# Performance work log

Measured on AMD Instinct MI355X. Metric: run time of the kernel, lower is better.

## Reference

```python
import jax, jax.numpy as jnp
import numpy as np

DECAY = 0.99
EPSILON = 1e-05
BETA = 0.25  # vq_commitment_beta


def setup_inputs() -> dict:
    key = jax.random.key(0)
    k1, k2, k3, k4 = jax.random.split(key, 4)
    N, dim, K = 32768, 512, 8192
    init_range = 1.0 / np.sqrt(dim)
    emb_w = jax.random.uniform(k3, (K, 2 * dim), dtype=jnp.float32,
                               minval=-init_range, maxval=init_range)
    return {
        "z_real": jax.random.normal(k1, (N, dim), dtype=jnp.float32),
        "z_imag": jax.random.normal(k2, (N, dim), dtype=jnp.float32),
        "emb_w": emb_w,
        "ema_cluster_size": jnp.zeros((K,), dtype=jnp.float32),
        "ema_w": emb_w.copy(),
    }


def reference(z_real, z_imag, emb_w, ema_cluster_size, ema_w):
    N, dim = z_real.shape
    K = emb_w.shape[0]
    z_flat = jnp.concatenate([z_real, z_imag], axis=-1)  # [N, 2*dim]

    # squared euclidean distances [N, K]
    x_sq = jnp.sum(z_flat * z_flat, axis=1, keepdims=True)
    y_sq = jnp.sum(emb_w * emb_w, axis=1)
    d = jnp.maximum(x_sq + y_sq - 2.0 * (z_flat @ emb_w.T), 0.0)
    indices = jnp.argmin(d, axis=-1)  # [N]
    z_q = emb_w[indices]              # [N, 2*dim]

    # EMA codebook update (training-mode buffer math, no grads)
    n_total = jnp.zeros((K,), z_flat.dtype).at[indices].add(1.0)
    new_cluster_size = ema_cluster_size * DECAY + (1.0 - DECAY) * n_total
    cs = new_cluster_size + EPSILON
    cs = cs + (cs < 1.0).astype(cs.dtype)
    dw = jnp.zeros((K, 2 * dim), z_flat.dtype).at[indices].add(z_flat)  # encodings.T @ z_flat
    new_ema_w = ema_w * DECAY + (1.0 - DECAY) * dw
    new_w = jnp.clip(new_ema_w / cs[:, None], -5.0, 5.0)

    loss_sample = BETA * jnp.mean((z_q - z_flat) ** 2, axis=-1)  # [N]

    # straight-through (forward value == z_q)
    z_q_st = z_flat + jax.lax.stop_gradient(z_q - z_flat)

    probs = n_total / N
    norm_entropy = -jnp.sum(probs * jnp.log(probs + 1e-10)) / np.log(float(K))

    z_q_r = z_q_st[..., :dim]
    z_q_i = z_q_st[..., dim:]
    return (z_q_r, z_q_i, loss_sample, indices, norm_entropy,
            new_w, new_cluster_size, new_ema_w)
```

## Files before the change

### kernel.cpp

```cpp
#include <hip/hip_runtime.h>
#include <hip/hip_bf16.h>

#define NROWS 32768
#define DIM   512
#define D2    1024
#define KCODE 8192
#define DECAYF 0.99f
#define OMD    0.01f
#define CANDCAP 16
#define ZMAX 6.0f
#define IRANGE 0.04419417382415922f
#define MARGIN_P (9200 << 7)

typedef __attribute__((ext_vector_type(4))) int   v4i;
typedef __attribute__((ext_vector_type(16))) int  i32x16;

#define WS_EMB8T   0u
#define WS_YSQ     8388608u
#define WS_NINT    8421376u
#define WS_ENT     8454144u
#define WS_FIDX    10682384u
#define WS_OFF     10813456u
#define WS_CUR     10846224u
#define WS_ROWLIST 10878992u

#define OUT_ZQR  0
#define OUT_ZQI  16777216
#define OUT_LOSS 33554432
#define OUT_IDX  33587200
#define OUT_ENT  33619968
#define OUT_NEWW 33619969
#define OUT_NCS  42008577
#define OUT_NEMA 42016769
#define PAIRS_OFF (OUT_NEWW + 1)

__device__ __forceinline__ float wredf(float v) {
    #pragma unroll
    for (int o = 32; o > 0; o >>= 1) v += __shfl_down(v, o, 64);
    return v;
}

__device__ __forceinline__ double wredd(double v) {
    #pragma unroll
    for (int o = 32; o > 0; o >>= 1) v += __shfl_down(v, o, 64);
    return __shfl(v, 0, 64);
}

__device__ __forceinline__ double ulp32_of(double v) {
    return scalbn(1.0, ilogb(v) - 23);
}

__device__ __forceinline__ void gload_lds16(const void* g, void* l) {
    __builtin_amdgcn_global_load_lds(
        (const __attribute__((address_space(1))) unsigned int*)(g),
        (__attribute__((address_space(3))) unsigned int*)(l), 16, 0, 0);
}

__device__ __forceinline__ int q4(float4 v, float s) {
    int a = (int)rintf(fminf(fmaxf(v.x * s, -127.f), 127.f));
    int b = (int)rintf(fminf(fmaxf(v.y * s, -127.f), 127.f));
    int c = (int)rintf(fminf(fmaxf(v.z * s, -127.f), 127.f));
    int d = (int)rintf(fminf(fmaxf(v.w * s, -127.f), 127.f));
    return (a & 255) | ((b & 255) << 8) | ((c & 255) << 16) | ((d & 255) << 24);
}

__global__ __launch_bounds__(256) void prep_emb(const float* __restrict__ emb,
                                                char* __restrict__ emb8t,
                                                int* __restrict__ ysq) {
    int wave = threadIdx.x >> 6, lane = threadIdx.x & 63;
    int k = blockIdx.x * 4 + wave;
    const float4* src = (const float4*)(emb + (size_t)k * D2);
    const float es = 127.0f / IRANGE;
    const float sfac_inv = 1.0f / (2.0f * (ZMAX / 127.0f) * (IRANGE / 127.0f));
    float s = 0.f;
    float4 v0 = src[lane * 4 + 0];
    float4 v1 = src[lane * 4 + 1];
    float4 v2 = src[lane * 4 + 2];
    float4 v3 = src[lane * 4 + 3];
    s += v0.x*v0.x + v0.y*v0.y + v0.z*v0.z + v0.w*v0.w;
    s += v1.x*v1.x + v1.y*v1.y + v1.z*v1.z + v1.w*v1.w;
    s += v2.x*v2.x + v2.y*v2.y + v2.z*v2.z + v2.w*v2.w;
    s += v3.x*v3.x + v3.y*v3.y + v3.z*v3.z + v3.w*v3.w;
    v4i pk; pk[0] = q4(v0, es); pk[1] = q4(v1, es); pk[2] = q4(v2, es); pk[3] = q4(v3, es);
    v4i* dst = (v4i*)(emb8t + (size_t)(k >> 5) * 32768 + (size_t)lane * 512 + (k & 31) * 16);
    *dst = pk;
    s = wredf(s);
    if (lane == 0) ysq[k] = (int)rintf(s * sfac_inv);
}

__global__ __launch_bounds__(256, 2) void argmin_gemm(
    const float* __restrict__ zr, const float* __restrict__ zi,
    const char* __restrict__ emb8t, const int* __restrict__ ysq,
    long long* __restrict__ pairs)
{
    __shared__ char bufs[2][32768];
    const int tid  = threadIdx.x;
    const int wave = tid >> 6, lane = tid & 63;
    const int colc = lane & 31;
    const int hh   = lane >> 5;
    const int rowblk = blockIdx.x >> 1;
    const int slice  = blockIdx.x & 1;

    const int arow = rowblk * 128 + wave * 32 + colc;
    const float zs = 127.0f / ZMAX;
    const float* zrp = zr + (size_t)arow * 512 + hh * 16;
    const float* zip = zi + (size_t)arow * 512 + hh * 16;
    v4i afrag[32];
    #pragma unroll
    for (int ft = 0; ft < 16; ++ft) {
        const float4* p = (const float4*)(zrp + ft * 32);
        v4i a; a[0] = q4(p[0], zs); a[1] = q4(p[1], zs); a[2] = q4(p[2], zs); a[3] = q4(p[3], zs);
        afrag[ft] = a;
    }
    #pragma unroll
    for (int ft = 0; ft < 16; ++ft) {
        const float4* p = (const float4*)(zip + ft * 32);
        v4i a; a[0] = q4(p[0], zs); a[1] = q4(p[1], zs); a[2] = q4(p[2], zs); a[3] = q4(p[3], zs);
        afrag[16 + ft] = a;
    }

    int tv0[16], tv1[16];
    #pragma unroll
    for (int g = 0; g < 16; ++g) { tv0[g] = 0x7FFFFFFF; tv1[g] = 0x7FFFFFFF; }

    const char* gslice = emb8t + (size_t)slice * 128 * 32768;
    const int* yslice = ysq + slice * 4096;

#define STAGE(dstbuf, t_) do {                                                   \
        const char* gb = gslice + (size_t)(t_) * 32768 + wave * 8192             \
                       + (size_t)lane * 16;                                      \
        char* lb = (dstbuf) + wave * 8192;                                       \
        _Pragma("unroll")                                                        \
        for (int q = 0; q < 8; ++q)                                              \
            gload_lds16(gb + q * 1024, lb + q * 1024);                           \
    } while (0)

    const int boff = colc * 16 + hh * 512;

    STAGE(bufs[0], 0);
    __syncthreads();

    for (int c = 0; c < 128; ++c) {
        const int cur = c & 1;
        if (c + 1 < 128) STAGE(bufs[cur ^ 1], c + 1);
        int ysv = yslice[c * 32 + colc];

        const char* bb = &bufs[cur][0] + boff;
        i32x16 accP, accQ;
        #pragma unroll
        for (int g = 0; g < 16; ++g) { accP[g] = 0; accQ[g] = 0; }
        __builtin_amdgcn_s_setprio(1);
        #pragma unroll
        for (int m = 0; m < 16; ++m) {
            v4i bP = *(const v4i*)(bb + (2 * m) * 1024);
            v4i bQ = *(const v4i*)(bb + (2 * m + 1) * 1024);
            accP = __builtin_amdgcn_mfma_i32_32x32x32_i8(afrag[2 * m],     bP, accP, 0, 0, 0);
            accQ = __builtin_amdgcn_mfma_i32_32x32x32_i8(afrag[2 * m + 1], bQ, accQ, 0, 0, 0);
        }
        __builtin_amdgcn_s_setprio(0);

        #pragma unroll
        for (int g = 0; g < 16; ++g) {
            int pk = ((ysv - accP[g] - accQ[g]) << 7) | c;
            tv1[g] = min(tv1[g], max(pk, tv0[g]));
            tv0[g] = min(tv0[g], pk);
        }
        __syncthreads();
    }
#undef STAGE

    #pragma unroll
    for (int g = 0; g < 16; ++g) {
        int rloc = (g & 3) + 8 * (g >> 2) + 4 * hh;
        int rowg = rowblk * 128 + wave * 32 + rloc;
        size_t base = (size_t)rowg * 128 + slice * 64 + colc * 2;
        int t0 = tv0[g], t1 = tv1[g];
        int code0 = slice * 4096 + (t0 & 127) * 32 + colc;
        int code1 = slice * 4096 + (t1 & 127) * 32 + colc;
        pairs[base + 0] = ((long long)(unsigned)code0 << 32) | (unsigned)t0;
        pairs[base + 1] = ((long long)(unsigned)code1 << 32) | (unsigned)t1;
    }
}

__global__ __launch_bounds__(256) void cleanup(
    const float* __restrict__ zr, const float* __restrict__ zi,
    const float* __restrict__ emb, const long long* __restrict__ pairs,
    int* __restrict__ fidx, int* __restrict__ nint, float* __restrict__ out)
{
    __shared__ int candlds[4][CANDCAP];
    int wave = threadIdx.x >> 6, lane = threadIdx.x & 63;
    int r = blockIdx.x * 4 + wave;

    const long long* pr = pairs + (size_t)r * 128;
    long long p0 = pr[lane];
    long long p1 = pr[64 + lane];
    int v0v = (int)(unsigned)p0;
    int i0  = (int)(p0 >> 32);
    int v1v = (int)(unsigned)p1;
    int i1  = (int)(p1 >> 32);
    int m = min(v0v, v1v);
    #pragma unroll
    for (int o = 32; o > 0; o >>= 1) m = min(m, __shfl_xor(m, o, 64));
    int lim = m + MARGIN_P;
    unsigned long long m0 = __ballot(v0v < lim);
    unsigned long long m1 = __ballot(v1v < lim);
    int t0 = __popcll(m0);
    int cnt = t0 + __popcll(m1);
    if (cnt > CANDCAP) cnt = CANDCAP;
    unsigned long long below = (lane == 63) ? 0xFFFFFFFFFFFFFFFFull >> 1
                                            : ((1ull << lane) - 1);
    if (v0v < lim) {
        int pos = __popcll(m0 & below);
        if (pos < CANDCAP) candlds[wave][pos] = i0;
    }
    if (v1v < lim) {
        int pos = t0 + __popcll(m1 & below);
        if (pos < CANDCAP) candlds[wave][pos] = i1;
    }
    int best = candlds[wave][0];

    float zreg[16];
    #pragma unroll
    for (int p = 0; p < 4; ++p) {
        int d4 = p * 64 + lane;
        const float4* zp = (d4 < 128) ? (const float4*)(zr + (size_t)r * 512)
                                      : ((const float4*)(zi + (size_t)r * 512) - 128);
        float4 zv = zp[d4];
        zreg[p * 4 + 0] = zv.x; zreg[p * 4 + 1] = zv.y;
        zreg[p * 4 + 2] = zv.z; zreg[p * 4 + 3] = zv.w;
    }

    if (cnt > 1) {
        double xs = 0.0;
        #pragma unroll
        for (int j = 0; j < 16; ++j) xs += (double)zreg[j] * (double)zreg[j];
        xs = wredd(xs);
        double uS = ulp32_of(xs);

        double bD = 1e300; int bi = 1 << 30;
        for (int i = 0; i < cnt; ++i) {
            int cdx = candlds[wave][i];
            const float4* ep = (const float4*)(emb + (size_t)cdx * 1024);
            double ys = 0.0, tt = 0.0;
            #pragma unroll
            for (int p = 0; p < 4; ++p) {
                float4 ev = ep[p * 64 + lane];
                float q0 = ev.x * ev.x, q1 = ev.y * ev.y, q2 = ev.z * ev.z, q3 = ev.w * ev.w;
                ys += (double)q0 + (double)q1 + (double)q2 + (double)q3;
                tt += (double)zreg[p * 4 + 0] * (double)ev.x
                    + (double)zreg[p * 4 + 1] * (double)ev.y
                    + (double)zreg[p * 4 + 2] * (double)ev.z
                    + (double)zreg[p * 4 + 3] * (double)ev.w;
            }
            ys = wredd(ys);
            tt = wredd(tt);
            float y32 = (float)ys;
            float t32 = (float)tt;
            double dex = xs + ys - 2.0 * tt;
            double ud = ulp32_of(dex);
            double D = rint((double)y32 / uS) * uS - rint(2.0 * (double)t32 / ud) * ud;
            if (D < bD || (D == bD && cdx < bi)) { bD = D; bi = cdx; }
        }
        best = bi;
    }

    const float4* ep = (const float4*)(emb + (size_t)best * 1024);
    float acc = 0.f;
    #pragma unroll
    for (int p = 0; p < 4; ++p) {
        int d4 = p * 64 + lane;
        float4 ev = ep[d4];
        float dx = ev.x - zreg[p * 4 + 0]; acc += dx * dx;
        float dy = ev.y - zreg[p * 4 + 1]; acc += dy * dy;
        float dz = ev.z - zreg[p * 4 + 2]; acc += dz * dz;
        float dw = ev.w - zreg[p * 4 + 3]; acc += dw * dw;
        float4* op = (d4 < 128) ? (float4*)(out + OUT_ZQR + (size_t)r * 512)
                                : ((float4*)(out + OUT_ZQI + (size_t)r * 512) - 128);
        op[d4] = ev;
    }
    acc = wredf(acc);
    if (lane == 0) {
        fidx[r] = best;
        out[OUT_IDX + r] = (float)best;
        out[OUT_LOSS + r] = 0.25f * acc * (1.f / 1024.f);
        atomicAdd(nint + best, 1);
    }
}

__global__ __launch_bounds__(256) void scan_codes(const int* __restrict__ nint,
                                                  int* __restrict__ off,
                                                  int* __restrict__ cur) {
    __shared__ int part[256];
    int tid = threadIdx.x;
    int base = tid * 32;
    int loc[32];
    int s = 0;
    #pragma unroll
    for (int j = 0; j < 32; ++j) { loc[j] = s; s += nint[base + j]; }
    part[tid] = s;
    __syncthreads();
    for (int o = 1; o < 256; o <<= 1) {
        int t = (tid >= o) ? part[tid - o] : 0;
        __syncthreads();
        part[tid] += t;
        __syncthreads();
    }
    int excl = part[tid] - s;
    #pragma unroll
    for (int j = 0; j < 32; ++j) {
        off[base + j] = excl + loc[j];
        cur[base + j] = 0;
    }
}

__global__ __launch_bounds__(256) void fill_rows(const int* __restrict__ fidx,
                                                 const int* __restrict__ off,
                                                 int* __restrict__ cur,
                                                 int* __restrict__ rowlist) {
    int r = blockIdx.x * 256 + threadIdx.x;
    int idx = fidx[r];
    int pos = atomicAdd(cur + idx, 1);
    rowlist[off[idx] + pos] = r;
}

__global__ __launch_bounds__(256) void ema_update(
    const float* __restrict__ zr, const float* __restrict__ zi,
    const float* __restrict__ emaw, const float* __restrict__ emacs,
    const int* __restrict__ nint, const int* __restrict__ off,
    const int* __restrict__ rowlist, float* __restrict__ out,
    float* __restrict__ entacc)
{
    int k = blockIdx.x;
    int tid = threadIdx.x;
    int cnt = nint[k];
    int o0 = off[k];
    float ax = 0.f, ay = 0.f, az = 0.f, aw = 0.f;
    for (int i = 0; i < cnt; ++i) {
        int r = rowlist[o0 + i];
        float4 zv = (tid < 128) ? ((const float4*)(zr + (size_t)r * 512))[tid]
                                : ((const float4*)(zi + (size_t)r * 512))[tid - 128];
        ax += zv.x; ay += zv.y; az += zv.z; aw += zv.w;
    }
    float4 ew = ((const float4*)(emaw + (size_t)k * 1024))[tid];
    float4 nem;
    nem.x = DECAYF * ew.x + OMD * ax;
    nem.y = DECAYF * ew.y + OMD * ay;
    nem.z = DECAYF * ew.z + OMD * az;
    nem.w = DECAYF * ew.w + OMD * aw;
    ((float4*)(out + OUT_NEMA + (size_t)k * 1024))[tid] = nem;
    float ncs = DECAYF * emacs[k] + OMD * (float)cnt;
    float cs = ncs + 1e-5f;
    if (cs < 1.f) cs += 1.f;
    float inv = 1.f / cs;
    float4 w;
    w.x = fminf(fmaxf(nem.x * inv, -5.f), 5.f);
    w.y = fminf(fmaxf(nem.y * inv, -5.f), 5.f);
    w.z = fminf(fmaxf(nem.z * inv, -5.f), 5.f);
    w.w = fminf(fmaxf(nem.w * inv, -5.f), 5.f);
    ((float4*)(out + OUT_NEWW + (size_t)k * 1024))[tid] = w;
    if (tid == 0) {
        out[OUT_NCS + k] = ncs;
        float p = (float)cnt / 32768.f;
        atomicAdd(entacc, -p * logf(p + 1e-10f));
    }
}

__global__ void ent_fin(const float* __restrict__ entacc, float* __restrict__ out) {
    if (threadIdx.x == 0) out[OUT_ENT] = entacc[0] / logf(8192.f);
}

extern "C" void kernel_launch(void* const* d_in, const int* in_sizes, int n_in,
                              void* d_out, int out_size, void* d_ws, size_t ws_size,
                              hipStream_t stream)
{
    const float* zr    = (const float*)d_in[0];
    const float* zi    = (const float*)d_in[1];
    const float* emb   = (const float*)d_in[2];
    const float* emacs = (const float*)d_in[3];
    const float* emaw  = (const float*)d_in[4];
    float* out = (float*)d_out;
    char* ws = (char*)d_ws;

    char*  emb8t   = (char*)(ws + WS_EMB8T);
    int*   ysq     = (int*)(ws + WS_YSQ);
    int*   nint    = (int*)(ws + WS_NINT);
    float* entacc  = (float*)(ws + WS_ENT);
    int*   fidx    = (int*)(ws + WS_FIDX);
    int*   off     = (int*)(ws + WS_OFF);
    int*   cur     = (int*)(ws + WS_CUR);
    int*   rowlist = (int*)(ws + WS_ROWLIST);
    long long* pairs = (long long*)(out + PAIRS_OFF);

    hipMemsetAsync(ws + WS_NINT, 0, 32768 + 16, stream);

    prep_emb   <<<2048, 256, 0, stream>>>(emb, emb8t, ysq);
    argmin_gemm<<<512,  256, 0, stream>>>(zr, zi, emb8t, ysq, pairs);
    cleanup    <<<8192, 256, 0, stream>>>(zr, zi, emb, pairs, fidx, nint, out);
    scan_codes <<<1,    256, 0, stream>>>(nint, off, cur);
    fill_rows  <<<128,  256, 0, stream>>>(fidx, off, cur, rowlist);
    ema_update <<<8192, 256, 0, stream>>>(zr, zi, emaw, emacs, nint, off, rowlist, out, entacc);
    ent_fin    <<<1,    64,  0, stream>>>(entacc, out);
}
```

Before: 545.5 us.

## Double rows per wave in int8 argmin GEMM and fold memset into prep

Each wave now handles 64 query rows (two 32-row A fragments) against every staged codebook tile, so each LDS B read feeds twice as many MFMAs. The grid halves to 256 blocks and launch bounds drop to one block per CU to make room for the doubled A fragments, accumulators and top-2 trackers. The separate memset of the count and entropy buffers is folded into prep_emb, removing one launch. The cost is heavy register pressure and only 256 blocks, which may leave CUs underused or cause spills.

```diff
diff --git a/kernel.cpp b/kernel.cpp
--- a/kernel.cpp
+++ b/kernel.cpp
@@ -66,7 +66,12 @@
 
 __global__ __launch_bounds__(256) void prep_emb(const float* __restrict__ emb,
                                                 char* __restrict__ emb8t,
-                                                int* __restrict__ ysq) {
+                                                int* __restrict__ ysq,
+                                                int* __restrict__ nint,
+                                                float* __restrict__ entacc) {
+    if (blockIdx.x < 32) nint[blockIdx.x * 256 + threadIdx.x] = 0;
+    else if (blockIdx.x == 32 && threadIdx.x == 0) entacc[0] = 0.f;
+
     int wave = threadIdx.x >> 6, lane = threadIdx.x & 63;
     int k = blockIdx.x * 4 + wave;
     const float4* src = (const float4*)(emb + (size_t)k * D2);
@@ -88,7 +93,7 @@
     if (lane == 0) ysq[k] = (int)rintf(s * sfac_inv);
 }
 
-__global__ __launch_bounds__(256, 2) void argmin_gemm(
+__global__ __launch_bounds__(256, 1) void argmin_gemm(
     const float* __restrict__ zr, const float* __restrict__ zi,
     const char* __restrict__ emb8t, const int* __restrict__ ysq,
     long long* __restrict__ pairs)
@@ -101,27 +106,49 @@
     const int rowblk = blockIdx.x >> 1;
     const int slice  = blockIdx.x & 1;
 
-    const int arow = rowblk * 128 + wave * 32 + colc;
+    const int arow0 = rowblk * 256 + wave * 64 + colc;
+    const int arow1 = arow0 + 32;
     const float zs = 127.0f / ZMAX;
-    const float* zrp = zr + (size_t)arow * 512 + hh * 16;
-    const float* zip = zi + (size_t)arow * 512 + hh * 16;
-    v4i afrag[32];
-    #pragma unroll
-    for (int ft = 0; ft < 16; ++ft) {
-        const float4* p = (const float4*)(zrp + ft * 32);
-        v4i a; a[0] = q4(p[0], zs); a[1] = q4(p[1], zs); a[2] = q4(p[2], zs); a[3] = q4(p[3], zs);
-        afrag[ft] = a;
-    }
-    #pragma unroll
-    for (int ft = 0; ft < 16; ++ft) {
-        const float4* p = (const float4*)(zip + ft * 32);
-        v4i a; a[0] = q4(p[0], zs); a[1] = q4(p[1], zs); a[2] = q4(p[2], zs); a[3] = q4(p[3], zs);
-        afrag[16 + ft] = a;
-    }
-
-    int tv0[16], tv1[16];
-    #pragma unroll
-    for (int g = 0; g < 16; ++g) { tv0[g] = 0x7FFFFFFF; tv1[g] = 0x7FFFFFFF; }
+    v4i afrag0[32], afrag1[32];
+    {
+        const float* zrp = zr + (size_t)arow0 * 512 + hh * 16;
+        const float* zip = zi + (size_t)arow0 * 512 + hh * 16;
+        #pragma unroll
+        for (int ft = 0; ft < 16; ++ft) {
+            const float4* p = (const float4*)(zrp + ft * 32);
+            v4i a; a[0] = q4(p[0], zs); a[1] = q4(p[1], zs); a[2] = q4(p[2], zs); a[3] = q4(p[3], zs);
+            afrag0[ft] = a;
+        }
+        #pragma unroll
+        for (int ft = 0; ft < 16; ++ft) {
+            const float4* p = (const float4*)(zip + ft * 32);
+            v4i a; a[0] = q4(p[0], zs); a[1] = q4(p[1], zs); a[2] = q4(p[2], zs); a[3] = q4(p[3], zs);
+            afrag0[16 + ft] = a;
+        }
+    }
+    {
+        const float* zrp = zr + (size_t)arow1 * 512 + hh * 16;
+        const float* zip = zi + (size_t)arow1 * 512 + hh * 16;
+        #pragma unroll
+        for (int ft = 0; ft < 16; ++ft) {
+            const float4* p = (const float4*)(zrp + ft * 32);
+            v4i a; a[0] = q4(p[0], zs); a[1] = q4(p[1], zs); a[2] = q4(p[2], zs); a[3] = q4(p[3], zs);
+            afrag1[ft] = a;
+        }
+        #pragma unroll
+        for (int ft = 0; ft < 16; ++ft) {
+            const float4* p = (const float4*)(zip + ft * 32);
+            v4i a; a[0] = q4(p[0], zs); a[1] = q4(p[1], zs); a[2] = q4(p[2], zs); a[3] = q4(p[3], zs);
+            afrag1[16 + ft] = a;
+        }
+    }
+
+    int tv00[16], tv01[16], tv10[16], tv11[16];
+    #pragma unroll
+    for (int g = 0; g < 16; ++g) {
+        tv00[g] = 0x7FFFFFFF; tv01[g] = 0x7FFFFFFF;
+        tv10[g] = 0x7FFFFFFF; tv11[g] = 0x7FFFFFFF;
+    }
 
     const char* gslice = emb8t + (size_t)slice * 128 * 32768;
     const int* yslice = ysq + slice * 4096;
@@ -146,24 +173,29 @@
         int ysv = yslice[c * 32 + colc];
 
         const char* bb = &bufs[cur][0] + boff;
-        i32x16 accP, accQ;
-        #pragma unroll
-        for (int g = 0; g < 16; ++g) { accP[g] = 0; accQ[g] = 0; }
+        i32x16 acc0P, acc0Q, acc1P, acc1Q;
+        #pragma unroll
+        for (int g = 0; g < 16; ++g) { acc0P[g] = 0; acc0Q[g] = 0; acc1P[g] = 0; acc1Q[g] = 0; }
         __builtin_amdgcn_s_setprio(1);
         #pragma unroll
         for (int m = 0; m < 16; ++m) {
             v4i bP = *(const v4i*)(bb + (2 * m) * 1024);
             v4i bQ = *(const v4i*)(bb + (2 * m + 1) * 1024);
-            accP = __builtin_amdgcn_mfma_i32_32x32x32_i8(afrag[2 * m],     bP, accP, 0, 0, 0);
-            accQ = __builtin_amdgcn_mfma_i32_32x32x32_i8(afrag[2 * m + 1], bQ, accQ, 0, 0, 0);
+            acc0P = __builtin_amdgcn_mfma_i32_32x32x32_i8(afrag0[2 * m],     bP, acc0P, 0, 0, 0);
+            acc1P = __builtin_amdgcn_mfma_i32_32x32x32_i8(afrag1[2 * m],     bP, acc1P, 0, 0, 0);
+            acc0Q = __builtin_amdgcn_mfma_i32_32x32x32_i8(afrag0[2 * m + 1], bQ, acc0Q, 0, 0, 0);
+            acc1Q = __builtin_amdgcn_mfma_i32_32x32x32_i8(afrag1[2 * m + 1], bQ, acc1Q, 0, 0, 0);
         }
         __builtin_amdgcn_s_setprio(0);
 
         #pragma unroll
         for (int g = 0; g < 16; ++g) {
-            int pk = ((ysv - accP[g] - accQ[g]) << 7) | c;
-            tv1[g] = min(tv1[g], max(pk, tv0[g]));
-            tv0[g] = min(tv0[g], pk);
+            int pk0 = ((ysv - acc0P[g] - acc0Q[g]) << 7) | c;
+            tv01[g] = min(tv01[g], max(pk0, tv00[g]));
+            tv00[g] = min(tv00[g], pk0);
+            int pk1 = ((ysv - acc1P[g] - acc1Q[g]) << 7) | c;
+            tv11[g] = min(tv11[g], max(pk1, tv10[g]));
+            tv10[g] = min(tv10[g], pk1);
         }
         __syncthreads();
     }
@@ -172,13 +204,16 @@
     #pragma unroll
     for (int g = 0; g < 16; ++g) {
         int rloc = (g & 3) + 8 * (g >> 2) + 4 * hh;
-        int rowg = rowblk * 128 + wave * 32 + rloc;
-        size_t base = (size_t)rowg * 128 + slice * 64 + colc * 2;
-        int t0 = tv0[g], t1 = tv1[g];
-        int code0 = slice * 4096 + (t0 & 127) * 32 + colc;
-        int code1 = slice * 4096 + (t1 & 127) * 32 + colc;
-        pairs[base + 0] = ((long long)(unsigned)code0 << 32) | (unsigned)t0;
-        pairs[base + 1] = ((long long)(unsigned)code1 << 32) | (unsigned)t1;
+        int row0 = rowblk * 256 + wave * 64 + rloc;
+        int row1 = row0 + 32;
+        size_t base0 = (size_t)row0 * 128 + slice * 64 + colc * 2;
+        size_t base1 = (size_t)row1 * 128 + slice * 64 + colc * 2;
+        int a0 = tv00[g], a1 = tv01[g];
+        int b0 = tv10[g], b1 = tv11[g];
+        pairs[base0 + 0] = ((long long)(unsigned)(slice * 4096 + (a0 & 127) * 32 + colc) << 32) | (unsigned)a0;
+        pairs[base0 + 1] = ((long long)(unsigned)(slice * 4096 + (a1 & 127) * 32 + colc) << 32) | (unsigned)a1;
+        pairs[base1 + 0] = ((long long)(unsigned)(slice * 4096 + (b0 & 127) * 32 + colc) << 32) | (unsigned)b0;
+        pairs[base1 + 1] = ((long long)(unsigned)(slice * 4096 + (b1 & 127) * 32 + colc) << 32) | (unsigned)b1;
     }
 }
 
@@ -391,10 +426,8 @@
     int*   rowlist = (int*)(ws + WS_ROWLIST);
     long long* pairs = (long long*)(out + PAIRS_OFF);
 
-    hipMemsetAsync(ws + WS_NINT, 0, 32768 + 16, stream);
-
-    prep_emb   <<<2048, 256, 0, stream>>>(emb, emb8t, ysq);
-    argmin_gemm<<<512,  256, 0, stream>>>(zr, zi, emb8t, ysq, pairs);
+    prep_emb   <<<2048, 256, 0, stream>>>(emb, emb8t, ysq, nint, entacc);
+    argmin_gemm<<<256,  256, 0, stream>>>(zr, zi, emb8t, ysq, pairs);
     cleanup    <<<8192, 256, 0, stream>>>(zr, zi, emb, pairs, fidx, nint, out);
     scan_codes <<<1,    256, 0, stream>>>(nint, off, cur);
     fill_rows  <<<128,  256, 0, stream>>>(fidx, off, cur, rowlist);
```

After: 560.5 us. 2.7% more time.
